# Performance work log

Measured on AMD Instinct MI355X. Metric: run time of the kernel, lower is better.

The kernel has to match this reference:

```python
import jax, jax.numpy as jnp
import numpy as np

B, S, D, N_OPS = 16, 8192, 128, 4


def setup_inputs() -> dict:
    key = jax.random.key(0)
    k1, k2, k3 = jax.random.split(key, 3)
    x = jax.random.normal(k1, (B, S, D), dtype=jnp.float32)
    # candidate op parameters: 4 Linear(D, D) layers, stacked
    W = jax.random.normal(k2, (N_OPS, D, D), dtype=jnp.float32) * (1.0 / np.sqrt(D))
    b = jax.random.normal(k3, (N_OPS, D), dtype=jnp.float32) * 0.01
    # one-hot path selector buffer: weights[0] = 1.0 (as in MixModule.__init__)
    weights = jnp.zeros((N_OPS,), dtype=jnp.float32).at[0].set(1.0)
    return {"x": x, "W": W, "b": b, "weights": weights}


def reference(x, W, b, weights):
    # Faithful to the torch loop: compute EVERY candidate op(x), then the
    # weighted (one-hot) sum. outs: [B, S, n_ops, D]
    outs = jnp.einsum("bsd,ofd->bsof", x, W) + b[None, None, :, :]
    y = jnp.einsum("bsof,o->bsf", outs, weights)
    return y
```

## Files before the change

### kernel.cpp

```cpp
#include <hip/hip_runtime.h>
#include <hip/hip_bf16.h>

#define D 128
#define TPB 8
#define NBUF 5
#define TILE_BYTES (32 * D * 4)
#define ROWS_PER_BLOCK (32 * TPB)

typedef __attribute__((ext_vector_type(8))) short short8;
typedef __attribute__((ext_vector_type(4))) float float4_t;

typedef const __attribute__((address_space(1))) void g_void;
typedef __attribute__((address_space(3))) void l_void;

__global__ void combine_kernel(const float* __restrict__ W,
                               const float* __restrict__ b,
                               const float* __restrict__ wts,
                               __hip_bfloat16* __restrict__ Wc,
                               float* __restrict__ bc) {
    int idx = blockIdx.x * blockDim.x + threadIdx.x;
    float w0 = wts[0], w1 = wts[1], w2 = wts[2], w3 = wts[3];
    if (idx < D * D) {
        float v = w0 * W[idx] + w1 * W[D * D + idx]
                + w2 * W[2 * D * D + idx] + w3 * W[3 * D * D + idx];
        Wc[idx] = __float2bfloat16(v);
    }
    if (idx < D) {
        bc[idx] = w0 * b[idx] + w1 * b[D + idx] + w2 * b[2 * D + idx] + w3 * b[3 * D + idx];
    }
}

__device__ __forceinline__ short8 cvt8_bf16(float4_t a, float4_t b) {
    union { short8 s; __hip_bfloat16 h[8]; } u;
    u.h[0] = __float2bfloat16(a[0]);
    u.h[1] = __float2bfloat16(a[1]);
    u.h[2] = __float2bfloat16(a[2]);
    u.h[3] = __float2bfloat16(a[3]);
    u.h[4] = __float2bfloat16(b[0]);
    u.h[5] = __float2bfloat16(b[1]);
    u.h[6] = __float2bfloat16(b[2]);
    u.h[7] = __float2bfloat16(b[3]);
    return u.s;
}

__global__ __launch_bounds__(256, 1) void gemm_kernel(const float* __restrict__ x,
                                                      const __hip_bfloat16* __restrict__ Wc,
                                                      const float* __restrict__ bc,
                                                      float* __restrict__ y, int M) {
    __shared__ __align__(16) char Bs[NBUF * TILE_BYTES];

    const int tid  = threadIdx.x;
    const int lane = tid & 63;
    const int wave = tid >> 6;
    const int r    = lane & 15;
    const int quad = lane >> 4;
    const int hb   = wave & 1;
    const int ch   = wave >> 1;

    const int row0 = blockIdx.x * ROWS_PER_BLOCK;
    if (row0 >= M) return;
    const float* xblk = x + (size_t)row0 * D;

    short8 wf[4][4];
    #pragma unroll
    for (int f = 0; f < 4; f++)
        #pragma unroll
        for (int ks = 0; ks < 4; ks++)
            wf[f][ks] = *(const short8*)((const short*)Wc
                          + (ch * 64 + f * 16 + r) * D + ks * 32 + quad * 8);

    float4_t bias[4];
    #pragma unroll
    for (int f = 0; f < 4; f++)
        bias[f] = *(const float4_t*)(bc + ch * 64 + f * 16 + quad * 4);

    int dsoff[4][2];
    #pragma unroll
    for (int ks = 0; ks < 4; ks++)
        #pragma unroll
        for (int h = 0; h < 2; h++)
            dsoff[ks][h] = (hb * 16 + r) * 512
                         + (((ks * 8 + quad * 2 + h) ^ (r & 7)) << 4);

#define STAGE(t) {                                                              \
        const char* tb = (const char*)(xblk + (t) * 32 * D);                    \
        char* db = Bs + ((t) % NBUF) * TILE_BYTES;                              \
        _Pragma("unroll")                                                       \
        for (int g = 0; g < 4; g++) {                                           \
            int R  = g * 8 + (tid >> 5);                                        \
            int sl = tid & 31;                                                  \
            const char* src = tb + R * 512 + ((sl ^ (R & 7)) << 4);             \
            __builtin_amdgcn_global_load_lds((g_void*)src,                      \
                (l_void*)(db + g * 4096 + (tid >> 6) * 1024), 16, 0, 0);        \
        }                                                                       \
    }

    STAGE(0)
    STAGE(1)
    STAGE(2)

#define STEP(T, NW) {                                                           \
        if ((T) + 3 < TPB) STAGE((T) + 3)                                       \
        asm volatile("s_waitcnt vmcnt(%0)" :: "i"(NW) : "memory");              \
        __builtin_amdgcn_sched_barrier(0);                                      \
        __builtin_amdgcn_s_barrier();                                           \
        const char* buf = Bs + ((T) % NBUF) * TILE_BYTES;                       \
        short8 xf[4];                                                           \
        _Pragma("unroll")                                                       \
        for (int ks = 0; ks < 4; ks++) {                                        \
            float4_t a0 = *(const float4_t*)(buf + dsoff[ks][0]);               \
            float4_t a1 = *(const float4_t*)(buf + dsoff[ks][1]);               \
            xf[ks] = cvt8_bf16(a0, a1);                                         \
        }                                                                       \
        asm volatile("s_waitcnt lgkmcnt(0)" ::: "memory");                      \
        __builtin_amdgcn_sched_barrier(0);                                      \
        float4_t acc[4];                                                        \
        _Pragma("unroll")                                                       \
        for (int f = 0; f < 4; f++) acc[f] = bias[f];                           \
        _Pragma("unroll")                                                       \
        for (int ks = 0; ks < 4; ks++) {                                        \
            _Pragma("unroll")                                                   \
            for (int f = 0; f < 4; f++)                                         \
                acc[f] = __builtin_amdgcn_mfma_f32_16x16x32_bf16(               \
                    wf[f][ks], xf[ks], acc[f], 0, 0, 0);                        \
        }                                                                       \
        float* yp = y + (size_t)(row0 + (T) * 32 + hb * 16 + r) * D             \
                      + ch * 64 + quad * 4;                                     \
        _Pragma("unroll")                                                       \
        for (int f = 0; f < 4; f++)                                             \
            *(float4_t*)(yp + f * 16) = acc[f];                                 \
    }

    STEP(0, 12)
    STEP(1, 16)
    STEP(2, 20)
    STEP(3, 24)
    STEP(4, 24)
    STEP(5, 20)
    STEP(6, 16)
    STEP(7, 12)
#undef STEP
#undef STAGE
}

extern "C" void kernel_launch(void* const* d_in, const int* in_sizes, int n_in,
                              void* d_out, int out_size, void* d_ws, size_t ws_size,
                              hipStream_t stream) {
    const float* x   = (const float*)d_in[0];
    const float* W   = (const float*)d_in[1];
    const float* b   = (const float*)d_in[2];
    const float* wts = (const float*)d_in[3];
    float* y = (float*)d_out;

    __hip_bfloat16* Wc = (__hip_bfloat16*)d_ws;
    float* bc = (float*)((char*)d_ws + D * D * sizeof(__hip_bfloat16));

    combine_kernel<<<(D * D + 255) / 256, 256, 0, stream>>>(W, b, wts, Wc, bc);

    const int M = in_sizes[0] / D;
    gemm_kernel<<<M / ROWS_PER_BLOCK, 256, 0, stream>>>(x, Wc, bc, y, M);
}
```

Baseline: 126.6 us.

## Fuse weight combination into GEMM kernel and shrink LDS ring to three buffers

Drops the separate combine kernel. Each GEMM block now loads all four fp32 weight matrices and biases, forms the weighted sum in registers and converts it to bf16 itself, which removes one kernel launch and the workspace round trip. The LDS staging ring goes from five buffers with prefetch depth three to three buffers with depth two. A second barrier is added after the LDS reads so a buffer is not overwritten while still in use, and the vmcnt waits are retuned to match. In exchange, each block does redundant weight loads and FMAs, and the shallower prefetch gives less latency hiding.

```diff
diff --git a/kernel.cpp b/kernel.cpp
--- a/kernel.cpp
+++ b/kernel.cpp
@@ -3,7 +3,7 @@
 
 #define D 128
 #define TPB 8
-#define NBUF 5
+#define NBUF 3
 #define TILE_BYTES (32 * D * 4)
 #define ROWS_PER_BLOCK (32 * TPB)
 
@@ -12,23 +12,6 @@
 
 typedef const __attribute__((address_space(1))) void g_void;
 typedef __attribute__((address_space(3))) void l_void;
-
-__global__ void combine_kernel(const float* __restrict__ W,
-                               const float* __restrict__ b,
-                               const float* __restrict__ wts,
-                               __hip_bfloat16* __restrict__ Wc,
-                               float* __restrict__ bc) {
-    int idx = blockIdx.x * blockDim.x + threadIdx.x;
-    float w0 = wts[0], w1 = wts[1], w2 = wts[2], w3 = wts[3];
-    if (idx < D * D) {
-        float v = w0 * W[idx] + w1 * W[D * D + idx]
-                + w2 * W[2 * D * D + idx] + w3 * W[3 * D * D + idx];
-        Wc[idx] = __float2bfloat16(v);
-    }
-    if (idx < D) {
-        bc[idx] = w0 * b[idx] + w1 * b[D + idx] + w2 * b[2 * D + idx] + w3 * b[3 * D + idx];
-    }
-}
 
 __device__ __forceinline__ short8 cvt8_bf16(float4_t a, float4_t b) {
     union { short8 s; __hip_bfloat16 h[8]; } u;
@@ -44,8 +27,9 @@
 }
 
 __global__ __launch_bounds__(256, 1) void gemm_kernel(const float* __restrict__ x,
-                                                      const __hip_bfloat16* __restrict__ Wc,
-                                                      const float* __restrict__ bc,
+                                                      const float* __restrict__ W,
+                                                      const float* __restrict__ bvec,
+                                                      const float* __restrict__ wts,
                                                       float* __restrict__ y, int M) {
     __shared__ __align__(16) char Bs[NBUF * TILE_BYTES];
 
@@ -61,18 +45,35 @@
     if (row0 >= M) return;
     const float* xblk = x + (size_t)row0 * D;
 
+    const float w0 = wts[0], w1 = wts[1], w2 = wts[2], w3 = wts[3];
+
     short8 wf[4][4];
     #pragma unroll
-    for (int f = 0; f < 4; f++)
+    for (int f = 0; f < 4; f++) {
         #pragma unroll
-        for (int ks = 0; ks < 4; ks++)
-            wf[f][ks] = *(const short8*)((const short*)Wc
-                          + (ch * 64 + f * 16 + r) * D + ks * 32 + quad * 8);
+        for (int ks = 0; ks < 4; ks++) {
+            const float* p = W + (size_t)(ch * 64 + f * 16 + r) * D + ks * 32 + quad * 8;
+            float4_t a = w0 * *(const float4_t*)(p)
+                       + w1 * *(const float4_t*)(p + D * D)
+                       + w2 * *(const float4_t*)(p + 2 * D * D)
+                       + w3 * *(const float4_t*)(p + 3 * D * D);
+            float4_t b = w0 * *(const float4_t*)(p + 4)
+                       + w1 * *(const float4_t*)(p + D * D + 4)
+                       + w2 * *(const float4_t*)(p + 2 * D * D + 4)
+                       + w3 * *(const float4_t*)(p + 3 * D * D + 4);
+            wf[f][ks] = cvt8_bf16(a, b);
+        }
+    }
 
     float4_t bias[4];
     #pragma unroll
-    for (int f = 0; f < 4; f++)
-        bias[f] = *(const float4_t*)(bc + ch * 64 + f * 16 + quad * 4);
+    for (int f = 0; f < 4; f++) {
+        const float* q = bvec + ch * 64 + f * 16 + quad * 4;
+        bias[f] = w0 * *(const float4_t*)(q)
+                + w1 * *(const float4_t*)(q + D)
+                + w2 * *(const float4_t*)(q + 2 * D)
+                + w3 * *(const float4_t*)(q + 3 * D);
+    }
 
     int dsoff[4][2];
     #pragma unroll
@@ -97,10 +98,9 @@
 
     STAGE(0)
     STAGE(1)
-    STAGE(2)
 
 #define STEP(T, NW) {                                                           \
-        if ((T) + 3 < TPB) STAGE((T) + 3)                                       \
+        if ((T) + 2 < TPB) STAGE((T) + 2)                                       \
         asm volatile("s_waitcnt vmcnt(%0)" :: "i"(NW) : "memory");              \
         __builtin_amdgcn_sched_barrier(0);                                      \
         __builtin_amdgcn_s_barrier();                                           \
@@ -114,6 +114,7 @@
         }                                                                       \
         asm volatile("s_waitcnt lgkmcnt(0)" ::: "memory");                      \
         __builtin_amdgcn_sched_barrier(0);                                      \
+        __builtin_amdgcn_s_barrier();       \
         float4_t acc[4];                                                        \
         _Pragma("unroll")                                                       \
         for (int f = 0; f < 4; f++) acc[f] = bias[f];                           \
@@ -131,14 +132,14 @@
             *(float4_t*)(yp + f * 16) = acc[f];                                 \
     }
 
-    STEP(0, 12)
-    STEP(1, 16)
-    STEP(2, 20)
-    STEP(3, 24)
-    STEP(4, 24)
-    STEP(5, 20)
-    STEP(6, 16)
-    STEP(7, 12)
+    STEP(0, 8)
+    STEP(1, 12)
+    STEP(2, 16)
+    STEP(3, 16)
+    STEP(4, 16)
+    STEP(5, 16)
+    STEP(6, 12)
+    STEP(7, 8)
 #undef STEP
 #undef STAGE
 }
@@ -152,11 +153,8 @@
     const float* wts = (const float*)d_in[3];
     float* y = (float*)d_out;
 
-    __hip_bfloat16* Wc = (__hip_bfloat16*)d_ws;
-    float* bc = (float*)((char*)d_ws + D * D * sizeof(__hip_bfloat16));
-
-    combine_kernel<<<(D * D + 255) / 256, 256, 0, stream>>>(W, b, wts, Wc, bc);
+    (void)d_ws; (void)ws_size;
 
     const int M = in_sizes[0] / D;
-    gemm_kernel<<<M / ROWS_PER_BLOCK, 256, 0, stream>>>(x, Wc, bc, y, M);
+    gemm_kernel<<<M / ROWS_PER_BLOCK, 256, 0, stream>>>(x, W, b, wts, y, M);
 }
```

After: 145.2 us. 1.15x slower.

## Replace LDS-staged x tiles with direct per-wave register double-buffered loads

Applied to the files above, without the earlier changes.

Drops the shared-memory ring buffer filled by global_load_lds, along with the block-wide barriers. Each wave now loads its own 16-row x fragments straight into registers using inline-asm global_load_dwordx4, double-buffered two tiles ahead and tracked with hand-set vmcnt counts. The wave-to-work mapping also changes: wave pairs cover 128-row groups and split the output columns. This removes LDS traffic and barriers, but each lane now issues more strided global loads and uses more VGPRs. It also relies on exact vmcnt accounting, including the stores, for correctness.

```diff
diff --git a/kernel.cpp b/kernel.cpp
--- a/kernel.cpp
+++ b/kernel.cpp
@@ -2,16 +2,11 @@
 #include <hip/hip_bf16.h>
 
 #define D 128
-#define TPB 8
-#define NBUF 5
-#define TILE_BYTES (32 * D * 4)
-#define ROWS_PER_BLOCK (32 * TPB)
+#define TPW 8
+#define ROWS_PER_BLOCK 256
 
 typedef __attribute__((ext_vector_type(8))) short short8;
 typedef __attribute__((ext_vector_type(4))) float float4_t;
-
-typedef const __attribute__((address_space(1))) void g_void;
-typedef __attribute__((address_space(3))) void l_void;
 
 __global__ void combine_kernel(const float* __restrict__ W,
                                const float* __restrict__ b,
@@ -43,77 +38,65 @@
     return u.s;
 }
 
+#define GLOAD16(dst, p) \
+    asm volatile("global_load_dwordx4 %0, %1, off" : "=v"(dst) : "v"(p) : "memory")
+
 __global__ __launch_bounds__(256, 1) void gemm_kernel(const float* __restrict__ x,
                                                       const __hip_bfloat16* __restrict__ Wc,
                                                       const float* __restrict__ bc,
                                                       float* __restrict__ y, int M) {
-    __shared__ __align__(16) char Bs[NBUF * TILE_BYTES];
-
     const int tid  = threadIdx.x;
     const int lane = tid & 63;
     const int wave = tid >> 6;
     const int r    = lane & 15;
     const int quad = lane >> 4;
-    const int hb   = wave & 1;
-    const int ch   = wave >> 1;
+    const int rg   = wave >> 1;
+    const int chf  = wave & 1;
 
-    const int row0 = blockIdx.x * ROWS_PER_BLOCK;
-    if (row0 >= M) return;
-    const float* xblk = x + (size_t)row0 * D;
+    const int m0 = blockIdx.x * ROWS_PER_BLOCK + rg * 128;
+    if (m0 >= M) return;
 
     short8 wf[4][4];
     #pragma unroll
     for (int f = 0; f < 4; f++)
         #pragma unroll
-        for (int ks = 0; ks < 4; ks++)
-            wf[f][ks] = *(const short8*)((const short*)Wc
-                          + (ch * 64 + f * 16 + r) * D + ks * 32 + quad * 8);
+        for (int ks = 0; ks < 4; ks++) {
+            const short* wp = (const short*)Wc
+                + (chf * 64 + f * 16 + r) * D + ks * 32 + quad * 8;
+            GLOAD16(wf[f][ks], wp);
+        }
 
     float4_t bias[4];
     #pragma unroll
-    for (int f = 0; f < 4; f++)
-        bias[f] = *(const float4_t*)(bc + ch * 64 + f * 16 + quad * 4);
+    for (int f = 0; f < 4; f++) {
+        const float* bp = bc + chf * 64 + f * 16 + quad * 4;
+        GLOAD16(bias[f], bp);
+    }
 
-    int dsoff[4][2];
-    #pragma unroll
-    for (int ks = 0; ks < 4; ks++)
-        #pragma unroll
-        for (int h = 0; h < 2; h++)
-            dsoff[ks][h] = (hb * 16 + r) * 512
-                         + (((ks * 8 + quad * 2 + h) ^ (r & 7)) << 4);
+    const float* xl = x + (size_t)(m0 + r) * D + quad * 8;
 
-#define STAGE(t) {                                                              \
-        const char* tb = (const char*)(xblk + (t) * 32 * D);                    \
-        char* db = Bs + ((t) % NBUF) * TILE_BYTES;                              \
+    float4_t B0[8], B1[8];
+
+#define REFILL(BUF, t) {                                                        \
+        const float* tp = xl + (t) * 16 * D;                                    \
         _Pragma("unroll")                                                       \
-        for (int g = 0; g < 4; g++) {                                           \
-            int R  = g * 8 + (tid >> 5);                                        \
-            int sl = tid & 31;                                                  \
-            const char* src = tb + R * 512 + ((sl ^ (R & 7)) << 4);             \
-            __builtin_amdgcn_global_load_lds((g_void*)src,                      \
-                (l_void*)(db + g * 4096 + (tid >> 6) * 1024), 16, 0, 0);        \
+        for (int ks = 0; ks < 4; ks++) {                                        \
+            GLOAD16(BUF[2 * ks],     tp + ks * 32);                             \
+            GLOAD16(BUF[2 * ks + 1], tp + ks * 32 + 4);                         \
         }                                                                       \
     }
 
-    STAGE(0)
-    STAGE(1)
-    STAGE(2)
+    REFILL(B0, 0)
+    REFILL(B1, 1)
 
-#define STEP(T, NW) {                                                           \
-        if ((T) + 3 < TPB) STAGE((T) + 3)                                       \
+#define STEP(T, BUF, NW) {                                                      \
         asm volatile("s_waitcnt vmcnt(%0)" :: "i"(NW) : "memory");              \
         __builtin_amdgcn_sched_barrier(0);                                      \
-        __builtin_amdgcn_s_barrier();                                           \
-        const char* buf = Bs + ((T) % NBUF) * TILE_BYTES;                       \
         short8 xf[4];                                                           \
         _Pragma("unroll")                                                       \
-        for (int ks = 0; ks < 4; ks++) {                                        \
-            float4_t a0 = *(const float4_t*)(buf + dsoff[ks][0]);               \
-            float4_t a1 = *(const float4_t*)(buf + dsoff[ks][1]);               \
-            xf[ks] = cvt8_bf16(a0, a1);                                         \
-        }                                                                       \
-        asm volatile("s_waitcnt lgkmcnt(0)" ::: "memory");                      \
-        __builtin_amdgcn_sched_barrier(0);                                      \
+        for (int ks = 0; ks < 4; ks++)                                          \
+            xf[ks] = cvt8_bf16(BUF[2 * ks], BUF[2 * ks + 1]);                   \
+        if ((T) + 2 < TPW) REFILL(BUF, (T) + 2)                                 \
         float4_t acc[4];                                                        \
         _Pragma("unroll")                                                       \
         for (int f = 0; f < 4; f++) acc[f] = bias[f];                           \
@@ -124,23 +107,22 @@
                 acc[f] = __builtin_amdgcn_mfma_f32_16x16x32_bf16(               \
                     wf[f][ks], xf[ks], acc[f], 0, 0, 0);                        \
         }                                                                       \
-        float* yp = y + (size_t)(row0 + (T) * 32 + hb * 16 + r) * D             \
-                      + ch * 64 + quad * 4;                                     \
+        float* yp = y + (size_t)(m0 + (T) * 16 + r) * D + chf * 64 + quad * 4;  \
         _Pragma("unroll")                                                       \
         for (int f = 0; f < 4; f++)                                             \
             *(float4_t*)(yp + f * 16) = acc[f];                                 \
     }
 
-    STEP(0, 12)
-    STEP(1, 16)
-    STEP(2, 20)
-    STEP(3, 24)
-    STEP(4, 24)
-    STEP(5, 20)
-    STEP(6, 16)
-    STEP(7, 12)
+    STEP(0, B0, 8)
+    STEP(1, B1, 12)
+    STEP(2, B0, 16)
+    STEP(3, B1, 16)
+    STEP(4, B0, 16)
+    STEP(5, B1, 16)
+    STEP(6, B0, 16)
+    STEP(7, B1, 8)
 #undef STEP
-#undef STAGE
+#undef REFILL
 }
 
 extern "C" void kernel_launch(void* const* d_in, const int* in_sizes, int n_in,
```

Measured after the change: 131.1 us. 3.6% more time.
